# Kernel optimization log

Measured on AMD Instinct MI355X. Metric: run time of the kernel, lower is better.

## Reference

```python
import jax, jax.numpy as jnp
import numpy as np

H = 1024; NH = 16; L = 4; K = 128; N = 65536
ADIM_MOVE = 9; ADIM_TURN = 4; S = 2 * K + 2


def setup_inputs() -> dict:
    key = jax.random.key(0)
    ks = jax.random.split(key, 24)
    s = 0.02
    d = {}
    d['x'] = jax.random.normal(ks[0], (1, H), jnp.float32)
    d['memory_vectors'] = jax.random.normal(ks[1], (N, H), jnp.float32)
    d['memory_next_vectors'] = jax.random.normal(ks[2], (N, H), jnp.float32)
    d['memory_surprises'] = jax.random.uniform(ks[3], (N,), jnp.float32)
    d['memory_rewards'] = jax.random.normal(ks[4], (N,), jnp.float32)
    d['rand_noise'] = jax.random.uniform(ks[5], (N,), jnp.float32)
    d['action_idx_move'] = jax.random.randint(ks[6], (N,), 0, ADIM_MOVE)
    d['action_idx_turn'] = jax.random.randint(ks[7], (N,), 0, ADIM_TURN)
    d['start_token'] = jax.random.uniform(ks[8], (1, H)) * 2 - 1
    d['pos_emb'] = jax.random.uniform(ks[9], (S, H)) * 2 - 1
    d['in_proj_w'] = jax.random.normal(ks[10], (L, 3 * H, H)) * s
    d['in_proj_b'] = jnp.zeros((L, 3 * H))
    d['out_w'] = jax.random.normal(ks[11], (L, H, H)) * s
    d['out_b'] = jnp.zeros((L, H))
    d['ln1_w'] = jnp.ones((L, H)); d['ln1_b'] = jnp.zeros((L, H))
    d['ln2_w'] = jnp.ones((L, H)); d['ln2_b'] = jnp.zeros((L, H))
    d['ffn_w1'] = jax.random.normal(ks[12], (L, 4 * H, H)) * s
    d['ffn_b1'] = jnp.zeros((L, 4 * H))
    d['ffn_w2'] = jax.random.normal(ks[13], (L, H, 4 * H)) * s
    d['ffn_b2'] = jnp.zeros((L, H))
    d['act_move_w1'] = jax.random.normal(ks[14], (H, ADIM_MOVE)) * s
    d['act_move_b1'] = jnp.zeros((H,))
    d['act_move_w2'] = jax.random.normal(ks[15], (H, H)) * s
    d['act_move_b2'] = jnp.zeros((H,))
    d['act_turn_w1'] = jax.random.normal(ks[16], (H, ADIM_TURN)) * s
    d['act_turn_b1'] = jnp.zeros((H,))
    d['act_turn_w2'] = jax.random.normal(ks[17], (H, H)) * s
    d['act_turn_b2'] = jnp.zeros((H,))
    d['vh_w1'] = jax.random.normal(ks[18], (4 * H, H)) * s
    d['vh_b1'] = jnp.zeros((4 * H,))
    d['vh_w2'] = jax.random.normal(ks[19], (1, 4 * H)) * s
    d['vh_b2'] = jnp.zeros((1,))
    return d


def _get_scores(v):
    # tie-aware average rank / N (matches torch unique_consecutive logic)
    srt = jnp.sort(v)
    left = jnp.searchsorted(srt, v, side='left')
    right = jnp.searchsorted(srt, v, side='right')
    return ((left + right - 1).astype(v.dtype) / 2) / v.shape[0]


def _ln(x, w, b):
    m = x.mean(-1, keepdims=True)
    var = ((x - m) ** 2).mean(-1, keepdims=True)
    return (x - m) / jnp.sqrt(var + 1e-5) * w + b


def _gelu(x):
    return jax.nn.gelu(x, approximate=False)


def _mha(x, wqkv, bqkv, wo, bo, mask):
    dh = H // NH
    qkv = x @ wqkv.T + bqkv                      # [S, 3H]
    q, k, v = jnp.split(qkv, 3, axis=-1)
    q = q.reshape(-1, NH, dh); k = k.reshape(-1, NH, dh); v = v.reshape(-1, NH, dh)
    att = jnp.einsum('qhd,khd->hqk', q, k) / np.sqrt(dh).astype(np.float32)
    att = jax.nn.softmax(att + mask, axis=-1)
    o = jnp.einsum('hqk,khd->qhd', att, v).reshape(-1, H)
    return o @ wo.T + bo


def reference(x, memory_vectors, memory_next_vectors, memory_surprises, memory_rewards, rand_noise, action_idx_move, action_idx_turn, start_token, pos_emb, in_proj_w, in_proj_b, out_w, out_b, ln1_w, ln1_b, ln2_w, ln2_b, ffn_w1, ffn_b1, ffn_w2, ffn_b2, act_move_w1, act_move_b1, act_move_w2, act_move_b2, act_turn_w1, act_turn_b1, act_turn_w2, act_turn_b2, vh_w1, vh_b1, vh_w2, vh_b2):
    eps = 1e-8
    # ---- scoring (no_grad in original) ----
    xs = jax.lax.stop_gradient(x)
    xn = xs / jnp.maximum(jnp.linalg.norm(xs, axis=-1, keepdims=True), eps)
    mn = memory_vectors / jnp.maximum(jnp.linalg.norm(memory_vectors, axis=-1, keepdims=True), eps)
    sim = mn @ xn[0]                              # [N]
    scores = _get_scores(memory_surprises) ** 2 + _get_scores(sim) ** 2 + _get_scores(rand_noise) ** 2
    _, idx = jax.lax.top_k(scores, K)             # [K]
    # ---- gather memories + action one-hots ----
    sel = jax.lax.stop_gradient(memory_vectors[idx])   # [K, H]
    oh_move = jax.nn.one_hot(action_idx_move[idx], ADIM_MOVE, dtype=x.dtype)
    oh_turn = jax.nn.one_hot(action_idx_turn[idx], ADIM_TURN, dtype=x.dtype)
    av_move = _gelu(oh_move @ act_move_w1.T + act_move_b1) @ act_move_w2.T + act_move_b2
    av_turn = _gelu(oh_turn @ act_turn_w1.T + act_turn_b1) @ act_turn_w2.T + act_turn_b2
    av = (av_move + av_turn) / 2                  # mean over actions
    # interleave [v0, a0, v1, a1, ...], prepend start, append target
    vecs = jnp.stack((sel, av), axis=1).reshape(-1, H)
    vecs = jnp.concatenate((start_token, vecs, x), axis=0)   # [S, H]
    vecs = vecs + pos_emb
    mask = jnp.where(jnp.tril(jnp.ones((S, S), bool)), 0.0, -jnp.inf).astype(x.dtype)
    for l in range(L):
        vecs = vecs + _mha(_ln(vecs, ln1_w[l], ln1_b[l]), in_proj_w[l], in_proj_b[l], out_w[l], out_b[l], mask)
        h = _ln(vecs, ln2_w[l], ln2_b[l])
        vecs = vecs + _gelu(h @ ffn_w1[l].T + ffn_b1[l]) @ ffn_w2[l].T + ffn_b2[l]
    vidx = jnp.arange(K + 1) * 2 + 1
    vh_in = vecs[vidx]
    vp = _gelu(vh_in @ vh_w1.T + vh_b1) @ vh_w2.T + vh_b2   # [K+1, 1]
    sel_rewards = memory_rewards[idx]
    losses = (vp[:-1].ravel() - sel_rewards) ** 2            # mse, reduction='none'
    return (vecs[1:], memory_next_vectors[idx], vp[-1], losses, sel_rewards)
```

## Files before the change

kernel.cpp:

```cpp
#include <hip/hip_runtime.h>
#include <hip/hip_bf16.h>
#include <math.h>
#include <stdint.h>

typedef unsigned int u32;
typedef unsigned short u16;
typedef unsigned long long u64;

#define NM   65536
#define HD   1024
#define KS   128
#define SQ   258
#define NL   4
#define NBIN 65536
#define CCAP 2048

using bf16x8 = __attribute__((ext_vector_type(8))) short;
using f32x4v = __attribute__((ext_vector_type(4))) float;

struct Ctrl { u32 b1, above1, T, candcnt; };

static constexpr size_t A256(size_t x){ return (x + 255) & ~(size_t)255; }

constexpr size_t OFF_H3   = 0;
constexpr size_t OFF_C3   = OFF_H3 + (size_t)3*NBIN*4;
constexpr size_t OFF_HS   = OFF_C3 + (size_t)3*NBIN*4;
constexpr size_t ZERO_BYTES = OFF_HS + (size_t)NBIN*4;
constexpr size_t OFF_BS   = A256(ZERO_BYTES);
constexpr size_t OFF_BB   = A256(OFF_BS + 192*4);
constexpr size_t OFF_VPB  = A256(OFF_BB + 192*4);
constexpr size_t OFF_XN   = A256(OFF_VPB + 1024);
constexpr size_t OFF_P3   = A256(OFF_XN + (size_t)HD*4);
constexpr size_t OFF_K3   = A256(OFF_P3 + (size_t)3*(NBIN+1)*4);
constexpr size_t OFF_L3   = A256(OFF_K3 + (size_t)3*NM*4);
constexpr size_t OFF_KSC  = A256(OFF_L3 + (size_t)3*NM*4);
constexpr size_t OFF_CAND = A256(OFF_KSC + (size_t)NM*4);
constexpr size_t OFF_CTRL = A256(OFF_CAND + (size_t)CCAP*8);
constexpr size_t OFF_IDX  = A256(OFF_CTRL + 256);
constexpr size_t OFF_REW  = A256(OFF_IDX  + (size_t)KS*4);
constexpr size_t OFF_HM   = A256(OFF_REW  + (size_t)KS*4);
constexpr size_t OFF_HT   = A256(OFF_HM   + (size_t)KS*HD*2);
constexpr size_t OFF_VECS = A256(OFF_HT   + (size_t)KS*HD*2);
constexpr size_t OFF_LNB  = A256(OFF_VECS + (size_t)SQ*HD*4);
constexpr size_t OFF_QKV  = A256(OFF_LNB  + (size_t)SQ*HD*2);
constexpr size_t OFF_ATT  = A256(OFF_QKV  + (size_t)SQ*3*HD*4);
constexpr size_t OFF_FFH  = A256(OFF_ATT  + (size_t)SQ*HD*2);
constexpr size_t OFF_VHIN = A256(OFF_FFH  + (size_t)SQ*4*HD*2);
constexpr size_t OFF_WB   = A256(OFF_VHIN + (size_t)129*HD*2);
constexpr size_t NWELEM   = 56623104;
constexpr size_t OFF_PART = A256(OFF_WB + NWELEM*2);

constexpr size_t WB_IN = 0;
constexpr size_t WB_O  = WB_IN + (size_t)4*3*HD*HD;
constexpr size_t WB_F1 = WB_O  + (size_t)4*HD*HD;
constexpr size_t WB_F2 = WB_F1 + (size_t)4*4*HD*HD;
constexpr size_t WB_AM = WB_F2 + (size_t)4*4*HD*HD;
constexpr size_t WB_AT = WB_AM + (size_t)HD*HD;
constexpr size_t WB_VH = WB_AT + (size_t)HD*HD;

constexpr int OUT_NEXT = 257*HD;
constexpr int OUT_VP   = OUT_NEXT + KS*HD;
constexpr int OUT_LOSS = OUT_VP + 1;
constexpr int OUT_REWO = OUT_LOSS + KS;

__device__ __forceinline__ float gelu_f(float v){
  return 0.5f*v*(1.0f + erff(v*0.70710678118654752440f));
}

__device__ __forceinline__ u16 f2bf(float f){
  __hip_bfloat16 h = __float2bfloat16(f);
  u16 s;
  __builtin_memcpy(&s, &h, sizeof(u16));
  return s;
}

__device__ __forceinline__ u32 fkey(float v){
  u32 b = __float_as_uint(v);
  return (b >> 31) ? ~b : (b | 0x80000000u);
}

__device__ __forceinline__ void gload16(const u16* g, u16* l){
  __builtin_amdgcn_global_load_lds(
      (const __attribute__((address_space(1))) unsigned int*)g,
      (__attribute__((address_space(3))) unsigned int*)l, 16, 0, 0);
}

struct WSeg { const float* s; u16* d; u32 base4, end4; };
struct WCA { WSeg seg[7]; u32 tot4; };
__global__ __launch_bounds__(256) void k_wconv(WCA a){
  u32 i = blockIdx.x*256 + threadIdx.x;
  if(i >= a.tot4) return;
  #pragma unroll
  for(int j=0;j<7;++j){
    if(i < a.seg[j].end4){
      u32 off = i - a.seg[j].base4;
      float4 v = *(const float4*)&a.seg[j].s[(size_t)off*4];
      u16 r[4] = { f2bf(v.x), f2bf(v.y), f2bf(v.z), f2bf(v.w) };
      u64 pk; __builtin_memcpy(&pk, r, 8);
      *(u64*)&a.seg[j].d[(size_t)off*4] = pk;
      return;
    }
  }
}

__global__ void k_xn(const float* __restrict__ x, float* __restrict__ xn){
  __shared__ float red[256];
  int t = threadIdx.x;
  float s = 0.f;
  for(int i=t;i<HD;i+=256){ float v=x[i]; s += v*v; }
  red[t]=s; __syncthreads();
  for(int o=128;o>0;o>>=1){ if(t<o) red[t]+=red[t+o]; __syncthreads(); }
  float nrm = fmaxf(sqrtf(red[0]), 1e-8f);
  for(int i=t;i<HD;i+=256) xn[i] = x[i]/nrm;
}

__global__ __launch_bounds__(256) void k_simkey(const float* __restrict__ mv, const float* __restrict__ xn,
                                                const float* __restrict__ surp, const float* __restrict__ noise,
                                                u32* __restrict__ keys3, u32* __restrict__ hist3){
  __shared__ float xs[HD];
  int t = threadIdx.x;
  for(int i=t;i<HD;i+=256) xs[i]=xn[i];
  __syncthreads();
  int lane = t & 63, w = t >> 6;
  int row = blockIdx.x*4 + w;
  const float4* p = (const float4*)(mv + (size_t)row*HD);
  const float4* q = (const float4*)xs;
  float d=0.f, ss=0.f;
  #pragma unroll
  for(int r=0;r<4;++r){
    float4 v = p[lane + 64*r]; float4 u = q[lane + 64*r];
    d  += v.x*u.x + v.y*u.y + v.z*u.z + v.w*u.w;
    ss += v.x*v.x + v.y*v.y + v.z*v.z + v.w*v.w;
  }
  for(int off=32;off>0;off>>=1){ d += __shfl_xor(d,off,64); ss += __shfl_xor(ss,off,64); }
  if(lane==0){
    float sim = d / fmaxf(sqrtf(ss),1e-8f);
    float vals[3] = { surp[row], sim, noise[row] };
    #pragma unroll
    for(int a=0;a<3;++a){
      u32 k = fkey(vals[a]);
      keys3[(size_t)a*NM + row] = k;
      atomicAdd(&hist3[(size_t)a*NBIN + (k >> 16)], 1u);
    }
  }
}

__global__ __launch_bounds__(256) void k_scanA(const u32* __restrict__ hist3, u32* __restrict__ bsum){
  __shared__ u32 red[256];
  int blk = blockIdx.x;
  int t = threadIdx.x;
  const u32* h = hist3 + (size_t)(blk>>6)*NBIN + (size_t)(blk&63)*1024;
  u32 s = 0;
  #pragma unroll
  for(int j=0;j<4;++j) s += h[t*4+j];
  red[t]=s; __syncthreads();
  for(int o=128;o>0;o>>=1){ if(t<o) red[t]+=red[t+o]; __syncthreads(); }
  if(t==0) bsum[blk] = red[0];
}

__global__ __launch_bounds__(256) void k_scanB(const u32* __restrict__ bsum, u32* __restrict__ bbase,
                                               u32* __restrict__ pref3){
  __shared__ u32 incl[256];
  int t = threadIdx.x;
  u32 v = (t < 192) ? bsum[t] : 0u;
  incl[t] = v; __syncthreads();
  for(int off=1;off<256;off<<=1){
    u32 u = (t >= off) ? incl[t-off] : 0u;
    __syncthreads(); incl[t] += u; __syncthreads();
  }
  if(t < 192){
    int a = t >> 6;
    u32 excl_t = incl[t] - v;
    u32 excl_a = incl[a*64] - bsum[a*64];
    bbase[t] = excl_t - excl_a;
  }
  if(t < 3) pref3[(size_t)t*(NBIN+1) + NBIN] = NM;
}

__global__ __launch_bounds__(256) void k_scanC(const u32* __restrict__ hist3, const u32* __restrict__ bbase,
                                               u32* __restrict__ pref3){
  __shared__ u32 part[256];
  int blk = blockIdx.x;
  int t = threadIdx.x;
  int a = blk >> 6, c = blk & 63;
  const u32* h = hist3 + (size_t)a*NBIN + (size_t)c*1024;
  u32* pref = pref3 + (size_t)a*(NBIN+1) + (size_t)c*1024;
  u32 loc[4]; u32 s = 0;
  #pragma unroll
  for(int j=0;j<4;++j){ loc[j] = h[t*4+j]; s += loc[j]; }
  part[t] = s; __syncthreads();
  for(int off=1;off<256;off<<=1){
    u32 u = (t >= off) ? part[t-off] : 0u;
    __syncthreads(); part[t] += u; __syncthreads();
  }
  u32 run = bbase[blk] + part[t] - s;
  #pragma unroll
  for(int j=0;j<4;++j){ pref[t*4+j] = run; run += loc[j]; }
}

__global__ void k_scatter3(const u32* __restrict__ keys3, const u32* __restrict__ pref3,
                           u32* __restrict__ cnt3, u32* __restrict__ lo3){
  int i = blockIdx.x*256 + threadIdx.x;
  if(i >= NM) return;
  #pragma unroll
  for(int a=0;a<3;++a){
    u32 k = keys3[(size_t)a*NM + i];
    u32 b = k >> 16;
    u32 pos = pref3[(size_t)a*(NBIN+1) + b] + atomicAdd(&cnt3[(size_t)a*NBIN + b], 1u);
    lo3[(size_t)a*NM + pos] = k & 0xFFFFu;
  }
}

__global__ void k_rank3score(const u32* __restrict__ keys3, const u32* __restrict__ pref3,
                             const u32* __restrict__ lo3, u32* __restrict__ keysS, u32* __restrict__ histS){
  int i = blockIdx.x*256 + threadIdx.x;
  if(i >= NM) return;
  float rr[3];
  #pragma unroll
  for(int a=0;a<3;++a){
    u32 k = keys3[(size_t)a*NM + i];
    u32 b = k >> 16, my = k & 0xFFFFu;
    const u32* pref = pref3 + (size_t)a*(NBIN+1);
    const u32* lo = lo3 + (size_t)a*NM;
    u32 s = pref[b], e = pref[b+1];
    u32 nl = 0, ne = 0;
    for(u32 j=s;j<e;++j){ u32 u = lo[j]; nl += (u < my); ne += (u == my); }
    u32 left = s + nl, right = left + ne;
    rr[a] = (float)(left + right - 1) * (1.0f/131072.0f);
  }
  float sc = __fadd_rn(__fadd_rn(__fmul_rn(rr[0],rr[0]), __fmul_rn(rr[1],rr[1])), __fmul_rn(rr[2],rr[2]));
  u32 k = __float_as_uint(sc);
  keysS[i] = k;
  atomicAdd(&histS[k >> 16], 1u);
}

__global__ __launch_bounds__(1024) void k_sel1(const u32* __restrict__ hist, Ctrl* ctrl){
  __shared__ u32 part[1024];
  int t = threadIdx.x;
  u32 base = t*64, s = 0;
  for(int j=0;j<64;++j) s += hist[base+j];
  part[t] = s; __syncthreads();
  for(int off=1;off<1024;off<<=1){
    u32 v = (t+off < 1024) ? part[t+off] : 0u;
    __syncthreads(); part[t] += v; __syncthreads();
  }
  u32 above = part[t] - s;
  if(above < (u32)KS && above + s >= (u32)KS){
    u32 cum = above;
    for(int j=63;j>=0;--j){
      u32 c = hist[base+j];
      if(cum + c >= (u32)KS){ ctrl->T = (u32)(base+j) << 16; ctrl->candcnt = 0; break; }
      cum += c;
    }
  }
}

__global__ void k_collect(const u32* __restrict__ keys, Ctrl* ctrl, u64* __restrict__ cand){
  int i = blockIdx.x*256 + threadIdx.x;
  if(i >= NM) return;
  u32 k = keys[i];
  if(k >= ctrl->T){
    u32 p = atomicAdd(&ctrl->candcnt, 1u);
    if(p < (u32)CCAP) cand[p] = ((u64)(~k) << 32) | (u32)i;
  }
}

__global__ __launch_bounds__(1024) void k_sortsel(const u64* __restrict__ cand, const Ctrl* ctrl, int* __restrict__ idx){
  __shared__ u64 sm[CCAP];
  int t = threadIdx.x;
  u32 n = ctrl->candcnt; if(n > (u32)CCAP) n = CCAP;
  for(int i=t;i<CCAP;i+=1024) sm[i] = (i < (int)n) ? cand[i] : 0xFFFFFFFFFFFFFFFFull;
  __syncthreads();
  for(int k=2;k<=CCAP;k<<=1){
    for(int j=k>>1;j>0;j>>=1){
      for(int i=t;i<CCAP;i+=1024){
        int ixj = i ^ j;
        if(ixj > i){
          bool up = ((i & k) == 0);
          u64 a = sm[i], b = sm[ixj];
          if((a > b) == up){ sm[i] = b; sm[ixj] = a; }
        }
      }
      __syncthreads();
    }
  }
  if(t < KS) idx[t] = (int)(sm[t] & 0xFFFFFFFFu);
}

__global__ void k_gather(const int* __restrict__ idx,
                         const float* __restrict__ mv, const float* __restrict__ mnv,
                         const float* __restrict__ mrew,
                         const int* __restrict__ aim, const int* __restrict__ ait,
                         const float* __restrict__ amw1, const float* __restrict__ amb1,
                         const float* __restrict__ atw1, const float* __restrict__ atb1,
                         const float* __restrict__ start, const float* __restrict__ x,
                         const float* __restrict__ pos,
                         float* __restrict__ vecs, float* __restrict__ outnext,
                         u16* __restrict__ hm, u16* __restrict__ ht,
                         float* __restrict__ rew, float* __restrict__ outrew){
  int k = blockIdx.x;
  int t = threadIdx.x;
  if(k < KS){
    int row = idx[k];
    const float* a = mv  + (size_t)row*HD;
    const float* b = mnv + (size_t)row*HD;
    const float* pz = pos + (size_t)(2*k+1)*HD;
    float* vr = vecs + (size_t)(2*k+1)*HD;
    for(int c=t;c<HD;c+=256){
      vr[c] = a[c] + pz[c];
      outnext[(size_t)k*HD+c] = b[c];
    }
    int am = aim[row], at = ait[row];
    for(int j=t;j<HD;j+=256){
      hm[(size_t)k*HD+j] = f2bf(gelu_f(amw1[(size_t)j*9 + am] + amb1[j]));
      ht[(size_t)k*HD+j] = f2bf(gelu_f(atw1[(size_t)j*4 + at] + atb1[j]));
    }
    if(t == 0){ float r = mrew[row]; rew[k] = r; outrew[k] = r; }
  } else {
    for(int c=t;c<HD;c+=256){
      vecs[c] = start[c] + pos[c];
      vecs[(size_t)(SQ-1)*HD + c] = x[c] + pos[(size_t)(SQ-1)*HD + c];
    }
  }
}

__device__ __forceinline__ void gemm_body(u16* As, u16* Bs, const u16* __restrict__ A, const u16* __restrict__ B,
        float* __restrict__ P, int M, int N, int K, int S, int nbm, int lda, int tile){
  int bm = (tile % nbm) * 64;
  int tmp = tile / nbm;
  int z  = tmp % S;
  int bn = (tmp / S) * 64;
  int Ks = K / S, kbeg = z*Ks;
  int nk = Ks >> 5;

  int t = threadIdx.x, lane = t & 63, w = t >> 6;
  int srow = w*16 + (lane >> 2);
  int clog = (lane & 3) ^ ((srow >> 1) & 3);
  const u16* ga = A + (size_t)(bm + srow)*lda + kbeg + clog*8;
  const u16* gb = B + (size_t)(bn + srow)*K  + kbeg + clog*8;
  u16* la = As + w*512;
  u16* lb = Bs + w*512;

  int wm = (w >> 1)*32, wn = (w & 1)*32;
  int lr = lane & 15, lg = lane >> 4;
  int r0 = wm + lr, r1 = r0 + 16;
  int c0 = wn + lr, c1 = c0 + 16;
  int aoff0 = r0*32 + ((lg ^ ((r0>>1)&3))*8);
  int aoff1 = r1*32 + ((lg ^ ((r1>>1)&3))*8);
  int boff0 = c0*32 + ((lg ^ ((c0>>1)&3))*8);
  int boff1 = c1*32 + ((lg ^ ((c1>>1)&3))*8);

  f32x4v acc00 = {0,0,0,0}, acc01 = {0,0,0,0}, acc10 = {0,0,0,0}, acc11 = {0,0,0,0};

  gload16(ga, la);
  gload16(gb, lb);
  ga += 32; gb += 32;
  __syncthreads();

  for(int kk = 0; kk < nk; ++kk){
    int cur = (kk & 1) * 2048;
    if(kk + 1 < nk){
      int nxt = 2048 - cur;
      gload16(ga, la + nxt);
      gload16(gb, lb + nxt);
      ga += 32; gb += 32;
    }
    bf16x8 a0 = *(const bf16x8*)&As[cur + aoff0];
    bf16x8 a1 = *(const bf16x8*)&As[cur + aoff1];
    bf16x8 b0 = *(const bf16x8*)&Bs[cur + boff0];
    bf16x8 b1 = *(const bf16x8*)&Bs[cur + boff1];
    acc00 = __builtin_amdgcn_mfma_f32_16x16x32_bf16(a0, b0, acc00, 0, 0, 0);
    acc01 = __builtin_amdgcn_mfma_f32_16x16x32_bf16(a0, b1, acc01, 0, 0, 0);
    acc10 = __builtin_amdgcn_mfma_f32_16x16x32_bf16(a1, b0, acc10, 0, 0, 0);
    acc11 = __builtin_amdgcn_mfma_f32_16x16x32_bf16(a1, b1, acc11, 0, 0, 0);
    __syncthreads();
  }

  size_t zbase = (size_t)z * (size_t)M;
  #pragma unroll
  for(int r=0;r<4;++r){
    int row0 = bm + wm + lg*4 + r;
    int row1 = row0 + 16;
    int cc0 = bn + wn + lr, cc1 = cc0 + 16;
    if(row0 < M){
      P[(zbase+row0)*N + cc0] = acc00[r];
      P[(zbase+row0)*N + cc1] = acc01[r];
    }
    if(row1 < M){
      P[(zbase+row1)*N + cc0] = acc10[r];
      P[(zbase+row1)*N + cc1] = acc11[r];
    }
  }
}

__global__ __launch_bounds__(256) void k_gemm(const u16* __restrict__ A, const u16* __restrict__ B,
        float* __restrict__ P, int M, int N, int K, int S, int nbm, int lda){
  __shared__ u16 As[4096];
  __shared__ u16 Bs[4096];
  u32 nwg = gridDim.x, orig = blockIdx.x;
  u32 swz = (orig & 7)*(nwg >> 3) + (orig >> 3);
  gemm_body(As, Bs, A, B, P, M, N, K, S, nbm, lda, (int)swz);
}

__global__ __launch_bounds__(256) void k_actgemm(const u16* __restrict__ hm, const u16* __restrict__ ht,
        const u16* __restrict__ amw2, const u16* __restrict__ atw2,
        float* __restrict__ part, float* __restrict__ part2){
  __shared__ u16 As[4096];
  __shared__ u16 Bs[4096];
  int which = blockIdx.x >> 8, tile = blockIdx.x & 255;
  gemm_body(As, Bs, which ? ht : hm, which ? atw2 : amw2, which ? part2 : part,
            KS, HD, HD, 8, 2, HD, tile);
}

template<int S_, int ACT, bool BF>
__global__ __launch_bounds__(256) void k_finS(const float* __restrict__ P, const float* __restrict__ bias,
                                              float* __restrict__ C, u16* __restrict__ Cb, int MN4, int Nd){
  int i4 = blockIdx.x*256 + threadIdx.x;
  if(i4 >= MN4) return;
  size_t off = (size_t)i4*4;
  size_t MN = (size_t)MN4*4;
  float4 v = *(const float4*)&P[off];
  #pragma unroll
  for(int z=1;z<S_;++z){
    float4 q = *(const float4*)&P[(size_t)z*MN + off];
    v.x += q.x; v.y += q.y; v.z += q.z; v.w += q.w;
  }
  int j = (i4 % (Nd/4))*4;
  float4 b4 = *(const float4*)&bias[j];
  v.x += b4.x; v.y += b4.y; v.z += b4.z; v.w += b4.w;
  if(ACT == 1){ v.x = gelu_f(v.x); v.y = gelu_f(v.y); v.z = gelu_f(v.z); v.w = gelu_f(v.w); }
  if(BF){
    u16 r[4] = { f2bf(v.x), f2bf(v.y), f2bf(v.z), f2bf(v.w) };
    u64 pk; __builtin_memcpy(&pk, r, 8);
    *(u64*)&Cb[off] = pk;
  } else {
    *(float4*)&C[off] = v;
  }
}

template<int S_, bool LN>
__global__ __launch_bounds__(256) void k_finrow(const float* __restrict__ P, const float* __restrict__ bias,
                                                float* __restrict__ vecs, const float* __restrict__ lw,
                                                const float* __restrict__ lb, u16* __restrict__ lnb,
                                                float* __restrict__ outp, u16* __restrict__ vhin){
  __shared__ float red[256];
  int row = blockIdx.x, t = threadIdx.x;
  int j = t*4;
  float4 v = *(const float4*)&P[(size_t)row*HD + j];
  #pragma unroll
  for(int z=1;z<S_;++z){
    float4 p = *(const float4*)&P[((size_t)z*SQ + row)*HD + j];
    v.x += p.x; v.y += p.y; v.z += p.z; v.w += p.w;
  }
  float4 b4 = *(const float4*)&bias[j];
  float4 r4 = *(const float4*)&vecs[(size_t)row*HD + j];
  v.x += b4.x + r4.x; v.y += b4.y + r4.y; v.z += b4.z + r4.z; v.w += b4.w + r4.w;
  *(float4*)&vecs[(size_t)row*HD + j] = v;
  if(LN){
    red[t] = v.x+v.y+v.z+v.w; __syncthreads();
    for(int o=128;o>0;o>>=1){ if(t<o) red[t]+=red[t+o]; __syncthreads(); }
    float m = red[0]*(1.0f/HD); __syncthreads();
    float dx=v.x-m, dy=v.y-m, dz=v.z-m, dw=v.w-m;
    red[t] = dx*dx+dy*dy+dz*dz+dw*dw; __syncthreads();
    for(int o=128;o>0;o>>=1){ if(t<o) red[t]+=red[t+o]; __syncthreads(); }
    float den = sqrtf(red[0]*(1.0f/HD) + 1e-5f);
    float4 w4 = *(const float4*)&lw[j];
    float4 lb4 = *(const float4*)&lb[j];
    u16 r[4] = { f2bf(dx/den*w4.x + lb4.x), f2bf(dy/den*w4.y + lb4.y),
                 f2bf(dz/den*w4.z + lb4.z), f2bf(dw/den*w4.w + lb4.w) };
    u64 pk; __builtin_memcpy(&pk, r, 8);
    *(u64*)&lnb[(size_t)row*HD + j] = pk;
  } else {
    if(row >= 1) *(float4*)&outp[(size_t)(row-1)*HD + j] = v;
    if(row & 1){
      int vr = (row-1) >> 1;
      u16 r[4] = { f2bf(v.x), f2bf(v.y), f2bf(v.z), f2bf(v.w) };
      u64 pk; __builtin_memcpy(&pk, r, 8);
      *(u64*)&vhin[(size_t)vr*HD + j] = pk;
    }
  }
}

__global__ __launch_bounds__(256) void k_finavln(const float* __restrict__ Pm, const float* __restrict__ Pt,
                                                 const float* __restrict__ bm_, const float* __restrict__ bt_,
                                                 const float* __restrict__ pos, float* __restrict__ vecs,
                                                 const float* __restrict__ lw, const float* __restrict__ lb,
                                                 u16* __restrict__ lnb){
  __shared__ float red[256];
  int row = blockIdx.x, t = threadIdx.x;
  int j = t*4;
  float4 v;
  if(row >= 2 && row <= 256 && ((row & 1) == 0)){
    int k = (row-2) >> 1;
    float4 s = {0,0,0,0};
    #pragma unroll
    for(int z=0;z<8;++z){
      float4 a = *(const float4*)&Pm[((size_t)z*KS + k)*HD + j];
      float4 b = *(const float4*)&Pt[((size_t)z*KS + k)*HD + j];
      s.x += a.x+b.x; s.y += a.y+b.y; s.z += a.z+b.z; s.w += a.w+b.w;
    }
    float4 bm4 = *(const float4*)&bm_[j];
    float4 bt4 = *(const float4*)&bt_[j];
    float4 p4 = *(const float4*)&pos[(size_t)row*HD + j];
    v.x = 0.5f*(s.x + bm4.x + bt4.x) + p4.x;
    v.y = 0.5f*(s.y + bm4.y + bt4.y) + p4.y;
    v.z = 0.5f*(s.z + bm4.z + bt4.z) + p4.z;
    v.w = 0.5f*(s.w + bm4.w + bt4.w) + p4.w;
    *(float4*)&vecs[(size_t)row*HD + j] = v;
  } else {
    v = *(const float4*)&vecs[(size_t)row*HD + j];
  }
  red[t] = v.x+v.y+v.z+v.w; __syncthreads();
  for(int o=128;o>0;o>>=1){ if(t<o) red[t]+=red[t+o]; __syncthreads(); }
  float m = red[0]*(1.0f/HD); __syncthreads();
  float dx=v.x-m, dy=v.y-m, dz=v.z-m, dw=v.w-m;
  red[t] = dx*dx+dy*dy+dz*dz+dw*dw; __syncthreads();
  for(int o=128;o>0;o>>=1){ if(t<o) red[t]+=red[t+o]; __syncthreads(); }
  float den = sqrtf(red[0]*(1.0f/HD) + 1e-5f);
  float4 w4 = *(const float4*)&lw[j];
  float4 lb4 = *(const float4*)&lb[j];
  u16 r[4] = { f2bf(dx/den*w4.x + lb4.x), f2bf(dy/den*w4.y + lb4.y),
               f2bf(dz/den*w4.z + lb4.z), f2bf(dw/den*w4.w + lb4.w) };
  u64 pk; __builtin_memcpy(&pk, r, 8);
  *(u64*)&lnb[(size_t)row*HD + j] = pk;
}

__global__ void k_attn(const float* __restrict__ qkv, u16* __restrict__ outp){
  __shared__ float qv[64];
  __shared__ float p[SQ];
  __shared__ float red[256];
  int q = blockIdx.x, h = blockIdx.y, t = threadIdx.x;
  if(t < 64) qv[t] = qkv[(size_t)q*3072 + h*64 + t];
  __syncthreads();
  int nk = q + 1;
  float lmax = -1e30f;
  for(int j=t;j<nk;j+=256){
    const float* kr = qkv + (size_t)j*3072 + 1024 + h*64;
    float d = 0.f;
    for(int c=0;c<64;++c) d += qv[c]*kr[c];
    d *= 0.125f;
    p[j] = d;
    lmax = fmaxf(lmax, d);
  }
  red[t] = lmax; __syncthreads();
  for(int o=128;o>0;o>>=1){ if(t<o) red[t] = fmaxf(red[t], red[t+o]); __syncthreads(); }
  float m = red[0];
  __syncthreads();
  float lsum = 0.f;
  for(int j=t;j<nk;j+=256){ float e = expf(p[j]-m); p[j] = e; lsum += e; }
  red[t] = lsum; __syncthreads();
  for(int o=128;o>0;o>>=1){ if(t<o) red[t] += red[t+o]; __syncthreads(); }
  float inv = 1.0f/red[0];
  __syncthreads();
  int d = t & 63, g = t >> 6;
  float acc = 0.f;
  for(int j=g;j<nk;j+=4) acc += p[j]*qkv[(size_t)j*3072 + 2048 + h*64 + d];
  red[t] = acc; __syncthreads();
  if(g == 0){
    float o4 = red[d] + red[64+d] + red[128+d] + red[192+d];
    outp[(size_t)q*HD + h*64 + d] = f2bf(o4*inv);
  }
}

__global__ __launch_bounds__(256) void k_vpfin(const float* __restrict__ P, const float* __restrict__ vb1,
                                               const float* __restrict__ vw2, float* __restrict__ vp){
  __shared__ float red[256];
  int r = blockIdx.x, t = threadIdx.x;
  float s = 0.f;
  for(int c=t;c<4096;c+=256){
    float v = P[(size_t)r*4096 + c];
    #pragma unroll
    for(int z=1;z<4;++z) v += P[((size_t)z*129 + r)*4096 + c];
    s += gelu_f(v + vb1[c]) * vw2[c];
  }
  red[t]=s; __syncthreads();
  for(int o=128;o>0;o>>=1){ if(t<o) red[t]+=red[t+o]; __syncthreads(); }
  if(t == 0) vp[r] = red[0];
}

__global__ void k_outsmall(const float* __restrict__ vp, const float* __restrict__ b2,
                           const float* __restrict__ rew, float* __restrict__ outp){
  int t = threadIdx.x;
  float bb = b2[0];
  if(t == 0) outp[OUT_VP] = vp[KS] + bb;
  if(t < KS){
    float d = (vp[t] + bb) - rew[t];
    outp[OUT_LOSS + t] = d*d;
    outp[OUT_REWO + t] = rew[t];
  }
}

extern "C" void kernel_launch(void* const* d_in, const int* in_sizes, int n_in,
                              void* d_out, int out_size, void* d_ws, size_t ws_size,
                              hipStream_t stream){
  const float* x     = (const float*)d_in[0];
  const float* mv    = (const float*)d_in[1];
  const float* mnv   = (const float*)d_in[2];
  const float* surp  = (const float*)d_in[3];
  const float* mrew  = (const float*)d_in[4];
  const float* noise = (const float*)d_in[5];
  const int*   aim   = (const int*)d_in[6];
  const int*   ait   = (const int*)d_in[7];
  const float* start = (const float*)d_in[8];
  const float* pos   = (const float*)d_in[9];
  const float* inW = (const float*)d_in[10]; const float* inB = (const float*)d_in[11];
  const float* oW  = (const float*)d_in[12]; const float* oB  = (const float*)d_in[13];
  const float* l1w = (const float*)d_in[14]; const float* l1b = (const float*)d_in[15];
  const float* l2w = (const float*)d_in[16]; const float* l2b = (const float*)d_in[17];
  const float* f1w = (const float*)d_in[18]; const float* f1b = (const float*)d_in[19];
  const float* f2w = (const float*)d_in[20]; const float* f2b = (const float*)d_in[21];
  const float* amw1= (const float*)d_in[22]; const float* amb1= (const float*)d_in[23];
  const float* amw2= (const float*)d_in[24]; const float* amb2= (const float*)d_in[25];
  const float* atw1= (const float*)d_in[26]; const float* atb1= (const float*)d_in[27];
  const float* atw2= (const float*)d_in[28]; const float* atb2= (const float*)d_in[29];
  const float* vw1 = (const float*)d_in[30]; const float* vb1 = (const float*)d_in[31];
  const float* vw2 = (const float*)d_in[32]; const float* vb2 = (const float*)d_in[33];

  float* out = (float*)d_out;
  char* ws = (char*)d_ws;
  u32*  hist3 = (u32*)(ws+OFF_H3);
  u32*  cnt3  = (u32*)(ws+OFF_C3);
  u32*  histS = (u32*)(ws+OFF_HS);
  u32*  bsum  = (u32*)(ws+OFF_BS);
  u32*  bbase = (u32*)(ws+OFF_BB);
  float* vp   = (float*)(ws+OFF_VPB);
  float* xn   = (float*)(ws+OFF_XN);
  u32*  pref3 = (u32*)(ws+OFF_P3);
  u32*  keys3 = (u32*)(ws+OFF_K3);
  u32*  lo3   = (u32*)(ws+OFF_L3);
  u32*  keysS = (u32*)(ws+OFF_KSC);
  u64*  cand  = (u64*)(ws+OFF_CAND);
  Ctrl* ctrl  = (Ctrl*)(ws+OFF_CTRL);
  int*  idxb  = (int*)(ws+OFF_IDX);
  float* rew  = (float*)(ws+OFF_REW);
  u16*  hm    = (u16*)(ws+OFF_HM);
  u16*  ht    = (u16*)(ws+OFF_HT);
  float* vecs = (float*)(ws+OFF_VECS);
  u16*  lnb   = (u16*)(ws+OFF_LNB);
  float* qkvb = (float*)(ws+OFF_QKV);
  u16*  attn  = (u16*)(ws+OFF_ATT);
  u16*  ffh   = (u16*)(ws+OFF_FFH);
  u16*  vhin  = (u16*)(ws+OFF_VHIN);
  u16*  wb    = (u16*)(ws+OFF_WB);
  float* part = (float*)(ws+OFF_PART);
  float* part2= part + (size_t)8*KS*HD;

  u16* inW_bf = wb + WB_IN;
  u16* oW_bf  = wb + WB_O;
  u16* f1w_bf = wb + WB_F1;
  u16* f2w_bf = wb + WB_F2;
  u16* am_bf  = wb + WB_AM;
  u16* at_bf  = wb + WB_AT;
  u16* vh_bf  = wb + WB_VH;

  dim3 b256(256);
  int gN = NM/256;

  (void)hipMemsetAsync(ws, 0, ZERO_BYTES, stream);

  {
    WCA a;
    const float* srcs[7] = { inW, oW, f1w, f2w, amw2, atw2, vw1 };
    u16* dsts[7] = { inW_bf, oW_bf, f1w_bf, f2w_bf, am_bf, at_bf, vh_bf };
    u32 sizes4[7] = { 4*3*HD*HD/4, 4*HD*HD/4, 4*4*HD*HD/4, 4*4*HD*HD/4, HD*HD/4, HD*HD/4, 4*HD*HD/4 };
    u32 cum = 0;
    for(int j=0;j<7;++j){
      a.seg[j].s = srcs[j]; a.seg[j].d = dsts[j];
      a.seg[j].base4 = cum; cum += sizes4[j]; a.seg[j].end4 = cum;
    }
    a.tot4 = cum;
    hipLaunchKernelGGL(k_wconv, dim3((cum + 255)/256), b256, 0, stream, a);
  }

  hipLaunchKernelGGL(k_xn, dim3(1), b256, 0, stream, x, xn);
  hipLaunchKernelGGL(k_simkey, dim3(NM/4), b256, 0, stream, mv, xn, surp, noise, keys3, hist3);
  hipLaunchKernelGGL(k_scanA, dim3(192), b256, 0, stream, hist3, bsum);
  hipLaunchKernelGGL(k_scanB, dim3(1), b256, 0, stream, bsum, bbase, pref3);
  hipLaunchKernelGGL(k_scanC, dim3(192), b256, 0, stream, hist3, bbase, pref3);
  hipLaunchKernelGGL(k_scatter3, dim3(gN), b256, 0, stream, keys3, pref3, cnt3, lo3);
  hipLaunchKernelGGL(k_rank3score, dim3(gN), b256, 0, stream, keys3, pref3, lo3, keysS, histS);
  hipLaunchKernelGGL(k_sel1, dim3(1), dim3(1024), 0, stream, histS, ctrl);
  hipLaunchKernelGGL(k_collect, dim3(gN), b256, 0, stream, keysS, ctrl, cand);
  hipLaunchKernelGGL(k_sortsel, dim3(1), dim3(1024), 0, stream, cand, ctrl, idxb);

  hipLaunchKernelGGL(k_gather, dim3(KS+1), b256, 0, stream, idxb, mv, mnv, mrew, aim, ait,
                     amw1, amb1, atw1, atb1, start, x, pos,
                     vecs, out + OUT_NEXT, hm, ht, rew, out + OUT_REWO);
  hipLaunchKernelGGL(k_actgemm, dim3(512), b256, 0, stream, hm, ht, am_bf, at_bf, part, part2);
  hipLaunchKernelGGL(k_finavln, dim3(SQ), b256, 0, stream, part, part2, amb2, atb2, pos, vecs, l1w, l1b, lnb);

  for(int l=0;l<NL;++l){
    hipLaunchKernelGGL(k_gemm, dim3(480), b256, 0, stream, lnb, inW_bf + (size_t)l*3*HD*HD, part, SQ, 3*HD, HD, 2, 5, HD);
    hipLaunchKernelGGL((k_finS<2,0,false>), dim3(774), b256, 0, stream, part, inB + (size_t)l*3*HD, qkvb, (u16*)nullptr, SQ*3*HD/4, 3*HD);
    hipLaunchKernelGGL(k_attn, dim3(SQ, 16), b256, 0, stream, qkvb, attn);
    hipLaunchKernelGGL(k_gemm, dim3(640), b256, 0, stream, attn, oW_bf + (size_t)l*HD*HD, part, SQ, HD, HD, 8, 5, HD);
    hipLaunchKernelGGL((k_finrow<8,true>), dim3(SQ), b256, 0, stream, part, oB + (size_t)l*HD, vecs,
                       l2w + (size_t)l*HD, l2b + (size_t)l*HD, lnb, (float*)nullptr, (u16*)nullptr);
    hipLaunchKernelGGL(k_gemm, dim3(640), b256, 0, stream, lnb, f1w_bf + (size_t)l*4*HD*HD, part, SQ, 4*HD, HD, 2, 5, HD);
    hipLaunchKernelGGL((k_finS<2,1,true>), dim3(1032), b256, 0, stream, part, f1b + (size_t)l*4*HD, (float*)nullptr, ffh, SQ*4*HD/4, 4*HD);
    hipLaunchKernelGGL(k_gemm, dim3(640), b256, 0, stream, ffh, f2w_bf + (size_t)l*HD*4*HD, part, SQ, HD, 4*HD, 8, 5, 4*HD);
    if(l < NL-1)
      hipLaunchKernelGGL((k_finrow<8,true>), dim3(SQ), b256, 0, stream, part, f2b + (size_t)l*HD, vecs,
                         l1w + (size_t)(l+1)*HD, l1b + (size_t)(l+1)*HD, lnb, (float*)nullptr, (u16*)nullptr);
    else
      hipLaunchKernelGGL((k_finrow<8,false>), dim3(SQ), b256, 0, stream, part, f2b + (size_t)l*HD, vecs,
                         (const float*)nullptr, (const float*)nullptr, (u16*)nullptr, out, vhin);
  }

  hipLaunchKernelGGL(k_gemm, dim3(768), b256, 0, stream, vhin, vh_bf, part, KS+1, 4*HD, HD, 4, 3, HD);
  hipLaunchKernelGGL(k_vpfin, dim3(KS+1), b256, 0, stream, part, vb1, vw2, vp);
  hipLaunchKernelGGL(k_outsmall, dim3(1), b256, 0, stream, vp, vb2, rew, out);
}
```

Before: 947.5 us.

## Fuse small kernels, store split-K partials and qkv in bf16, fold memset into wconv

Several small launches are merged: x-normalisation goes into simkey, scanB into scanC, sel1/collect/sortsel into one selection kernel, and outsmall into vpfin. The workspace memset is replaced by zeroing inside the weight-conversion kernel. Split-K GEMM partials and the qkv buffer are now stored as bf16 instead of fp32, roughly halving that memory traffic at the cost of extra rounding in the partial sums. The gather copies and simkey are also vectorised or processed two rows per wave.

```diff
diff --git a/kernel.cpp b/kernel.cpp
--- a/kernel.cpp
+++ b/kernel.cpp
@@ -18,32 +18,26 @@
 using bf16x8 = __attribute__((ext_vector_type(8))) short;
 using f32x4v = __attribute__((ext_vector_type(4))) float;
 
-struct Ctrl { u32 b1, above1, T, candcnt; };
-
 static constexpr size_t A256(size_t x){ return (x + 255) & ~(size_t)255; }
 
 constexpr size_t OFF_H3   = 0;
 constexpr size_t OFF_C3   = OFF_H3 + (size_t)3*NBIN*4;
 constexpr size_t OFF_HS   = OFF_C3 + (size_t)3*NBIN*4;
 constexpr size_t ZERO_BYTES = OFF_HS + (size_t)NBIN*4;
+constexpr u32 ZBLK = 1792;
 constexpr size_t OFF_BS   = A256(ZERO_BYTES);
-constexpr size_t OFF_BB   = A256(OFF_BS + 192*4);
-constexpr size_t OFF_VPB  = A256(OFF_BB + 192*4);
-constexpr size_t OFF_XN   = A256(OFF_VPB + 1024);
-constexpr size_t OFF_P3   = A256(OFF_XN + (size_t)HD*4);
+constexpr size_t OFF_P3   = A256(OFF_BS + 192*4);
 constexpr size_t OFF_K3   = A256(OFF_P3 + (size_t)3*(NBIN+1)*4);
 constexpr size_t OFF_L3   = A256(OFF_K3 + (size_t)3*NM*4);
 constexpr size_t OFF_KSC  = A256(OFF_L3 + (size_t)3*NM*4);
-constexpr size_t OFF_CAND = A256(OFF_KSC + (size_t)NM*4);
-constexpr size_t OFF_CTRL = A256(OFF_CAND + (size_t)CCAP*8);
-constexpr size_t OFF_IDX  = A256(OFF_CTRL + 256);
+constexpr size_t OFF_IDX  = A256(OFF_KSC + (size_t)NM*4);
 constexpr size_t OFF_REW  = A256(OFF_IDX  + (size_t)KS*4);
 constexpr size_t OFF_HM   = A256(OFF_REW  + (size_t)KS*4);
 constexpr size_t OFF_HT   = A256(OFF_HM   + (size_t)KS*HD*2);
 constexpr size_t OFF_VECS = A256(OFF_HT   + (size_t)KS*HD*2);
 constexpr size_t OFF_LNB  = A256(OFF_VECS + (size_t)SQ*HD*4);
 constexpr size_t OFF_QKV  = A256(OFF_LNB  + (size_t)SQ*HD*2);
-constexpr size_t OFF_ATT  = A256(OFF_QKV  + (size_t)SQ*3*HD*4);
+constexpr size_t OFF_ATT  = A256(OFF_QKV  + (size_t)SQ*3*HD*2);
 constexpr size_t OFF_FFH  = A256(OFF_ATT  + (size_t)SQ*HD*2);
 constexpr size_t OFF_VHIN = A256(OFF_FFH  + (size_t)SQ*4*HD*2);
 constexpr size_t OFF_WB   = A256(OFF_VHIN + (size_t)129*HD*2);
@@ -63,15 +57,34 @@
 constexpr int OUT_LOSS = OUT_VP + 1;
 constexpr int OUT_REWO = OUT_LOSS + KS;
 
+struct Ctrl { u32 b1, above1, T, candcnt; };
+
 __device__ __forceinline__ float gelu_f(float v){
   return 0.5f*v*(1.0f + erff(v*0.70710678118654752440f));
 }
 
 __device__ __forceinline__ u16 f2bf(float f){
   __hip_bfloat16 h = __float2bfloat16(f);
-  u16 s;
-  __builtin_memcpy(&s, &h, sizeof(u16));
+  u16 s; __builtin_memcpy(&s, &h, sizeof(u16));
   return s;
+}
+
+__device__ __forceinline__ float bf2f(u16 v){ return __uint_as_float(((u32)v) << 16); }
+
+__device__ __forceinline__ float4 unpk4(u64 pk){
+  u32 lo = (u32)pk, hi = (u32)(pk >> 32);
+  float4 v;
+  v.x = __uint_as_float(lo << 16);
+  v.y = __uint_as_float(lo & 0xFFFF0000u);
+  v.z = __uint_as_float(hi << 16);
+  v.w = __uint_as_float(hi & 0xFFFF0000u);
+  return v;
+}
+
+__device__ __forceinline__ u64 pk4(float4 v){
+  u16 r[4] = { f2bf(v.x), f2bf(v.y), f2bf(v.z), f2bf(v.w) };
+  u64 pk; __builtin_memcpy(&pk, r, 8);
+  return pk;
 }
 
 __device__ __forceinline__ u32 fkey(float v){
@@ -86,8 +99,9 @@
 }
 
 struct WSeg { const float* s; u16* d; u32 base4, end4; };
-struct WCA { WSeg seg[7]; u32 tot4; };
+struct WCA { WSeg seg[7]; u32 tot4; u32* z; };
 __global__ __launch_bounds__(256) void k_wconv(WCA a){
+  if(blockIdx.x < ZBLK) a.z[blockIdx.x*256 + threadIdx.x] = 0u;
   u32 i = blockIdx.x*256 + threadIdx.x;
   if(i >= a.tot4) return;
   #pragma unroll
@@ -95,15 +109,16 @@
     if(i < a.seg[j].end4){
       u32 off = i - a.seg[j].base4;
       float4 v = *(const float4*)&a.seg[j].s[(size_t)off*4];
-      u16 r[4] = { f2bf(v.x), f2bf(v.y), f2bf(v.z), f2bf(v.w) };
-      u64 pk; __builtin_memcpy(&pk, r, 8);
-      *(u64*)&a.seg[j].d[(size_t)off*4] = pk;
+      *(u64*)&a.seg[j].d[(size_t)off*4] = pk4(v);
       return;
     }
   }
 }
 
-__global__ void k_xn(const float* __restrict__ x, float* __restrict__ xn){
+__global__ __launch_bounds__(256) void k_simkey(const float* __restrict__ mv, const float* __restrict__ x,
+                                                const float* __restrict__ surp, const float* __restrict__ noise,
+                                                u32* __restrict__ keys3, u32* __restrict__ hist3){
+  __shared__ float xs[HD];
   __shared__ float red[256];
   int t = threadIdx.x;
   float s = 0.f;
@@ -111,36 +126,31 @@
   red[t]=s; __syncthreads();
   for(int o=128;o>0;o>>=1){ if(t<o) red[t]+=red[t+o]; __syncthreads(); }
   float nrm = fmaxf(sqrtf(red[0]), 1e-8f);
-  for(int i=t;i<HD;i+=256) xn[i] = x[i]/nrm;
-}
-
-__global__ __launch_bounds__(256) void k_simkey(const float* __restrict__ mv, const float* __restrict__ xn,
-                                                const float* __restrict__ surp, const float* __restrict__ noise,
-                                                u32* __restrict__ keys3, u32* __restrict__ hist3){
-  __shared__ float xs[HD];
-  int t = threadIdx.x;
-  for(int i=t;i<HD;i+=256) xs[i]=xn[i];
+  for(int i=t;i<HD;i+=256) xs[i] = x[i]/nrm;
   __syncthreads();
   int lane = t & 63, w = t >> 6;
-  int row = blockIdx.x*4 + w;
-  const float4* p = (const float4*)(mv + (size_t)row*HD);
-  const float4* q = (const float4*)xs;
-  float d=0.f, ss=0.f;
-  #pragma unroll
-  for(int r=0;r<4;++r){
-    float4 v = p[lane + 64*r]; float4 u = q[lane + 64*r];
-    d  += v.x*u.x + v.y*u.y + v.z*u.z + v.w*u.w;
-    ss += v.x*v.x + v.y*v.y + v.z*v.z + v.w*v.w;
-  }
-  for(int off=32;off>0;off>>=1){ d += __shfl_xor(d,off,64); ss += __shfl_xor(ss,off,64); }
-  if(lane==0){
-    float sim = d / fmaxf(sqrtf(ss),1e-8f);
-    float vals[3] = { surp[row], sim, noise[row] };
+  #pragma unroll
+  for(int rep=0;rep<2;++rep){
+    int row = blockIdx.x*8 + rep*4 + w;
+    const float4* p = (const float4*)(mv + (size_t)row*HD);
+    const float4* q = (const float4*)xs;
+    float d=0.f, ss=0.f;
     #pragma unroll
-    for(int a=0;a<3;++a){
-      u32 k = fkey(vals[a]);
-      keys3[(size_t)a*NM + row] = k;
-      atomicAdd(&hist3[(size_t)a*NBIN + (k >> 16)], 1u);
+    for(int r=0;r<4;++r){
+      float4 v = p[lane + 64*r]; float4 u = q[lane + 64*r];
+      d  += v.x*u.x + v.y*u.y + v.z*u.z + v.w*u.w;
+      ss += v.x*v.x + v.y*v.y + v.z*v.z + v.w*v.w;
+    }
+    for(int off=32;off>0;off>>=1){ d += __shfl_xor(d,off,64); ss += __shfl_xor(ss,off,64); }
+    if(lane==0){
+      float sim = d / fmaxf(sqrtf(ss),1e-8f);
+      float vals[3] = { surp[row], sim, noise[row] };
+      #pragma unroll
+      for(int a=0;a<3;++a){
+        u32 k = fkey(vals[a]);
+        keys3[(size_t)a*NM + row] = k;
+        atomicAdd(&hist3[(size_t)a*NBIN + (k >> 16)], 1u);
+      }
     }
   }
 }
@@ -158,31 +168,14 @@
   if(t==0) bsum[blk] = red[0];
 }
 
-__global__ __launch_bounds__(256) void k_scanB(const u32* __restrict__ bsum, u32* __restrict__ bbase,
-                                               u32* __restrict__ pref3){
-  __shared__ u32 incl[256];
-  int t = threadIdx.x;
-  u32 v = (t < 192) ? bsum[t] : 0u;
-  incl[t] = v; __syncthreads();
-  for(int off=1;off<256;off<<=1){
-    u32 u = (t >= off) ? incl[t-off] : 0u;
-    __syncthreads(); incl[t] += u; __syncthreads();
-  }
-  if(t < 192){
-    int a = t >> 6;
-    u32 excl_t = incl[t] - v;
-    u32 excl_a = incl[a*64] - bsum[a*64];
-    bbase[t] = excl_t - excl_a;
-  }
-  if(t < 3) pref3[(size_t)t*(NBIN+1) + NBIN] = NM;
-}
-
-__global__ __launch_bounds__(256) void k_scanC(const u32* __restrict__ hist3, const u32* __restrict__ bbase,
+__global__ __launch_bounds__(256) void k_scanC(const u32* __restrict__ hist3, const u32* __restrict__ bsum,
                                                u32* __restrict__ pref3){
   __shared__ u32 part[256];
   int blk = blockIdx.x;
   int t = threadIdx.x;
   int a = blk >> 6, c = blk & 63;
+  u32 base = 0;
+  for(int j=0;j<c;++j) base += bsum[a*64 + j];
   const u32* h = hist3 + (size_t)a*NBIN + (size_t)c*1024;
   u32* pref = pref3 + (size_t)a*(NBIN+1) + (size_t)c*1024;
   u32 loc[4]; u32 s = 0;
@@ -193,9 +186,10 @@
     u32 u = (t >= off) ? part[t-off] : 0u;
     __syncthreads(); part[t] += u; __syncthreads();
   }
-  u32 run = bbase[blk] + part[t] - s;
+  u32 run = base + part[t] - s;
   #pragma unroll
   for(int j=0;j<4;++j){ pref[t*4+j] = run; run += loc[j]; }
+  if(c == 63 && t == 255) pref3[(size_t)a*(NBIN+1) + NBIN] = NM;
 }
 
 __global__ void k_scatter3(const u32* __restrict__ keys3, const u32* __restrict__ pref3,
@@ -234,11 +228,14 @@
   atomicAdd(&histS[k >> 16], 1u);
 }
 
-__global__ __launch_bounds__(1024) void k_sel1(const u32* __restrict__ hist, Ctrl* ctrl){
+__global__ __launch_bounds__(1024) void k_selsort(const u32* __restrict__ histS, const u32* __restrict__ keysS,
+                                                  int* __restrict__ idx){
   __shared__ u32 part[1024];
+  __shared__ u64 sm[CCAP];
+  __shared__ u32 thrT, cnt;
   int t = threadIdx.x;
   u32 base = t*64, s = 0;
-  for(int j=0;j<64;++j) s += hist[base+j];
+  for(int j=0;j<64;++j) s += histS[base+j];
   part[t] = s; __syncthreads();
   for(int off=1;off<1024;off<<=1){
     u32 v = (t+off < 1024) ? part[t+off] : 0u;
@@ -248,28 +245,23 @@
   if(above < (u32)KS && above + s >= (u32)KS){
     u32 cum = above;
     for(int j=63;j>=0;--j){
-      u32 c = hist[base+j];
-      if(cum + c >= (u32)KS){ ctrl->T = (u32)(base+j) << 16; ctrl->candcnt = 0; break; }
+      u32 c = histS[base+j];
+      if(cum + c >= (u32)KS){ thrT = (u32)(base+j) << 16; cnt = 0; break; }
       cum += c;
     }
   }
-}
-
-__global__ void k_collect(const u32* __restrict__ keys, Ctrl* ctrl, u64* __restrict__ cand){
-  int i = blockIdx.x*256 + threadIdx.x;
-  if(i >= NM) return;
-  u32 k = keys[i];
-  if(k >= ctrl->T){
-    u32 p = atomicAdd(&ctrl->candcnt, 1u);
-    if(p < (u32)CCAP) cand[p] = ((u64)(~k) << 32) | (u32)i;
-  }
-}
-
-__global__ __launch_bounds__(1024) void k_sortsel(const u64* __restrict__ cand, const Ctrl* ctrl, int* __restrict__ idx){
-  __shared__ u64 sm[CCAP];
-  int t = threadIdx.x;
-  u32 n = ctrl->candcnt; if(n > (u32)CCAP) n = CCAP;
-  for(int i=t;i<CCAP;i+=1024) sm[i] = (i < (int)n) ? cand[i] : 0xFFFFFFFFFFFFFFFFull;
+  __syncthreads();
+  u32 T = thrT;
+  for(int i=t;i<NM;i+=1024){
+    u32 k = keysS[i];
+    if(k >= T){
+      u32 p = atomicAdd(&cnt, 1u);
+      if(p < (u32)CCAP) sm[p] = ((u64)(~k) << 32) | (u32)i;
+    }
+  }
+  __syncthreads();
+  u32 n = cnt; if(n > (u32)CCAP) n = CCAP;
+  for(int i=t;i<CCAP;i+=1024) if(i >= (int)n) sm[i] = 0xFFFFFFFFFFFFFFFFull;
   __syncthreads();
   for(int k=2;k<=CCAP;k<<=1){
     for(int j=k>>1;j>0;j>>=1){
@@ -302,14 +294,14 @@
   int t = threadIdx.x;
   if(k < KS){
     int row = idx[k];
-    const float* a = mv  + (size_t)row*HD;
-    const float* b = mnv + (size_t)row*HD;
-    const float* pz = pos + (size_t)(2*k+1)*HD;
-    float* vr = vecs + (size_t)(2*k+1)*HD;
-    for(int c=t;c<HD;c+=256){
-      vr[c] = a[c] + pz[c];
-      outnext[(size_t)k*HD+c] = b[c];
-    }
+    const float4* a = (const float4*)(mv  + (size_t)row*HD);
+    const float4* b = (const float4*)(mnv + (size_t)row*HD);
+    const float4* pz = (const float4*)(pos + (size_t)(2*k+1)*HD);
+    float4* vr = (float4*)(vecs + (size_t)(2*k+1)*HD);
+    float4* on = (float4*)(outnext + (size_t)k*HD);
+    float4 av = a[t], bv = b[t], pv = pz[t];
+    av.x += pv.x; av.y += pv.y; av.z += pv.z; av.w += pv.w;
+    vr[t] = av; on[t] = bv;
     int am = aim[row], at = ait[row];
     for(int j=t;j<HD;j+=256){
       hm[(size_t)k*HD+j] = f2bf(gelu_f(amw1[(size_t)j*9 + am] + amb1[j]));
@@ -317,15 +309,20 @@
     }
     if(t == 0){ float r = mrew[row]; rew[k] = r; outrew[k] = r; }
   } else {
-    for(int c=t;c<HD;c+=256){
-      vecs[c] = start[c] + pos[c];
-      vecs[(size_t)(SQ-1)*HD + c] = x[c] + pos[(size_t)(SQ-1)*HD + c];
-    }
+    const float4* st = (const float4*)start;
+    const float4* xx = (const float4*)x;
+    const float4* p0 = (const float4*)pos;
+    const float4* p1 = (const float4*)(pos + (size_t)(SQ-1)*HD);
+    float4 v0 = st[t], v1 = xx[t], q0 = p0[t], q1 = p1[t];
+    v0.x += q0.x; v0.y += q0.y; v0.z += q0.z; v0.w += q0.w;
+    v1.x += q1.x; v1.y += q1.y; v1.z += q1.z; v1.w += q1.w;
+    ((float4*)vecs)[t] = v0;
+    ((float4*)(vecs + (size_t)(SQ-1)*HD))[t] = v1;
   }
 }
 
 __device__ __forceinline__ void gemm_body(u16* As, u16* Bs, const u16* __restrict__ A, const u16* __restrict__ B,
-        float* __restrict__ P, int M, int N, int K, int S, int nbm, int lda, int tile){
+        u16* __restrict__ P, int M, int N, int K, int S, int nbm, int lda, int tile){
   int bm = (tile % nbm) * 64;
   int tmp = tile / nbm;
   int z  = tmp % S;
@@ -383,18 +380,18 @@
     int row1 = row0 + 16;
     int cc0 = bn + wn + lr, cc1 = cc0 + 16;
     if(row0 < M){
-      P[(zbase+row0)*N + cc0] = acc00[r];
-      P[(zbase+row0)*N + cc1] = acc01[r];
+      P[(zbase+row0)*N + cc0] = f2bf(acc00[r]);
+      P[(zbase+row0)*N + cc1] = f2bf(acc01[r]);
     }
     if(row1 < M){
-      P[(zbase+row1)*N + cc0] = acc10[r];
-      P[(zbase+row1)*N + cc1] = acc11[r];
+      P[(zbase+row1)*N + cc0] = f2bf(acc10[r]);
+      P[(zbase+row1)*N + cc1] = f2bf(acc11[r]);
     }
   }
 }
 
 __global__ __launch_bounds__(256) void k_gemm(const u16* __restrict__ A, const u16* __restrict__ B,
-        float* __restrict__ P, int M, int N, int K, int S, int nbm, int lda){
+        u16* __restrict__ P, int M, int N, int K, int S, int nbm, int lda){
   __shared__ u16 As[4096];
   __shared__ u16 Bs[4096];
   u32 nwg = gridDim.x, orig = blockIdx.x;
@@ -404,7 +401,7 @@
 
 __global__ __launch_bounds__(256) void k_actgemm(const u16* __restrict__ hm, const u16* __restrict__ ht,
         const u16* __restrict__ amw2, const u16* __restrict__ atw2,
-        float* __restrict__ part, float* __restrict__ part2){
+        u16* __restrict__ part, u16* __restrict__ part2){
   __shared__ u16 As[4096];
   __shared__ u16 Bs[4096];
   int which = blockIdx.x >> 8, tile = blockIdx.x & 255;
@@ -412,44 +409,39 @@
             KS, HD, HD, 8, 2, HD, tile);
 }
 
-template<int S_, int ACT, bool BF>
-__global__ __launch_bounds__(256) void k_finS(const float* __restrict__ P, const float* __restrict__ bias,
+template<int S_, int ACT, bool BFOUT>
+__global__ __launch_bounds__(256) void k_finS(const u16* __restrict__ P, const float* __restrict__ bias,
                                               float* __restrict__ C, u16* __restrict__ Cb, int MN4, int Nd){
   int i4 = blockIdx.x*256 + threadIdx.x;
   if(i4 >= MN4) return;
   size_t off = (size_t)i4*4;
   size_t MN = (size_t)MN4*4;
-  float4 v = *(const float4*)&P[off];
+  float4 v = unpk4(*(const u64*)&P[off]);
   #pragma unroll
   for(int z=1;z<S_;++z){
-    float4 q = *(const float4*)&P[(size_t)z*MN + off];
+    float4 q = unpk4(*(const u64*)&P[(size_t)z*MN + off]);
     v.x += q.x; v.y += q.y; v.z += q.z; v.w += q.w;
   }
   int j = (i4 % (Nd/4))*4;
   float4 b4 = *(const float4*)&bias[j];
   v.x += b4.x; v.y += b4.y; v.z += b4.z; v.w += b4.w;
   if(ACT == 1){ v.x = gelu_f(v.x); v.y = gelu_f(v.y); v.z = gelu_f(v.z); v.w = gelu_f(v.w); }
-  if(BF){
-    u16 r[4] = { f2bf(v.x), f2bf(v.y), f2bf(v.z), f2bf(v.w) };
-    u64 pk; __builtin_memcpy(&pk, r, 8);
-    *(u64*)&Cb[off] = pk;
-  } else {
-    *(float4*)&C[off] = v;
-  }
+  if(BFOUT) *(u64*)&Cb[off] = pk4(v);
+  else      *(float4*)&C[off] = v;
 }
 
 template<int S_, bool LN>
-__global__ __launch_bounds__(256) void k_finrow(const float* __restrict__ P, const float* __restrict__ bias,
+__global__ __launch_bounds__(256) void k_finrow(const u16* __restrict__ P, const float* __restrict__ bias,
                                                 float* __restrict__ vecs, const float* __restrict__ lw,
                                                 const float* __restrict__ lb, u16* __restrict__ lnb,
                                                 float* __restrict__ outp, u16* __restrict__ vhin){
   __shared__ float red[256];
   int row = blockIdx.x, t = threadIdx.x;
   int j = t*4;
-  float4 v = *(const float4*)&P[(size_t)row*HD + j];
+  float4 v = unpk4(*(const u64*)&P[(size_t)row*HD + j]);
   #pragma unroll
   for(int z=1;z<S_;++z){
-    float4 p = *(const float4*)&P[((size_t)z*SQ + row)*HD + j];
+    float4 p = unpk4(*(const u64*)&P[((size_t)z*SQ + row)*HD + j]);
     v.x += p.x; v.y += p.y; v.z += p.z; v.w += p.w;
   }
   float4 b4 = *(const float4*)&bias[j];
@@ -466,22 +458,20 @@
     float den = sqrtf(red[0]*(1.0f/HD) + 1e-5f);
     float4 w4 = *(const float4*)&lw[j];
     float4 lb4 = *(const float4*)&lb[j];
-    u16 r[4] = { f2bf(dx/den*w4.x + lb4.x), f2bf(dy/den*w4.y + lb4.y),
-                 f2bf(dz/den*w4.z + lb4.z), f2bf(dw/den*w4.w + lb4.w) };
-    u64 pk; __builtin_memcpy(&pk, r, 8);
-    *(u64*)&lnb[(size_t)row*HD + j] = pk;
+    float4 o4;
+    o4.x = dx/den*w4.x + lb4.x; o4.y = dy/den*w4.y + lb4.y;
+    o4.z = dz/den*w4.z + lb4.z; o4.w = dw/den*w4.w + lb4.w;
+    *(u64*)&lnb[(size_t)row*HD + j] = pk4(o4);
   } else {
     if(row >= 1) *(float4*)&outp[(size_t)(row-1)*HD + j] = v;
     if(row & 1){
       int vr = (row-1) >> 1;
-      u16 r[4] = { f2bf(v.x), f2bf(v.y), f2bf(v.z), f2bf(v.w) };
-      u64 pk; __builtin_memcpy(&pk, r, 8);
-      *(u64*)&vhin[(size_t)vr*HD + j] = pk;
-    }
-  }
-}
-
-__global__ __launch_bounds__(256) void k_finavln(const float* __restrict__ Pm, const float* __restrict__ Pt,
+      *(u64*)&vhin[(size_t)vr*HD + j] = pk4(v);
+    }
+  }
+}
+
+__global__ __launch_bounds__(256) void k_finavln(const u16* __restrict__ Pm, const u16* __restrict__ Pt,
                                                  const float* __restrict__ bm_, const float* __restrict__ bt_,
                                                  const float* __restrict__ pos, float* __restrict__ vecs,
                                                  const float* __restrict__ lw, const float* __restrict__ lb,
@@ -495,8 +485,8 @@
     float4 s = {0,0,0,0};
     #pragma unroll
     for(int z=0;z<8;++z){
-      float4 a = *(const float4*)&Pm[((size_t)z*KS + k)*HD + j];
-      float4 b = *(const float4*)&Pt[((size_t)z*KS + k)*HD + j];
+      float4 a = unpk4(*(const u64*)&Pm[((size_t)z*KS + k)*HD + j]);
+      float4 b = unpk4(*(const u64*)&Pt[((size_t)z*KS + k)*HD + j]);
       s.x += a.x+b.x; s.y += a.y+b.y; s.z += a.z+b.z; s.w += a.w+b.w;
     }
     float4 bm4 = *(const float4*)&bm_[j];
@@ -519,25 +509,30 @@
   float den = sqrtf(red[0]*(1.0f/HD) + 1e-5f);
   float4 w4 = *(const float4*)&lw[j];
   float4 lb4 = *(const float4*)&lb[j];
-  u16 r[4] = { f2bf(dx/den*w4.x + lb4.x), f2bf(dy/den*w4.y + lb4.y),
-               f2bf(dz/den*w4.z + lb4.z), f2bf(dw/den*w4.w + lb4.w) };
-  u64 pk; __builtin_memcpy(&pk, r, 8);
-  *(u64*)&lnb[(size_t)row*HD + j] = pk;
-}
-
-__global__ void k_attn(const float* __restrict__ qkv, u16* __restrict__ outp){
+  float4 o4;
+  o4.x = dx/den*w4.x + lb4.x; o4.y = dy/den*w4.y + lb4.y;
+  o4.z = dz/den*w4.z + lb4.z; o4.w = dw/den*w4.w + lb4.w;
+  *(u64*)&lnb[(size_t)row*HD + j] = pk4(o4);
+}
+
+__global__ void k_attn(const u16* __restrict__ qkv, u16* __restrict__ outp){
   __shared__ float qv[64];
   __shared__ float p[SQ];
   __shared__ float red[256];
   int q = blockIdx.x, h = blockIdx.y, t = threadIdx.x;
-  if(t < 64) qv[t] = qkv[(size_t)q*3072 + h*64 + t];
+  if(t < 64) qv[t] = bf2f(qkv[(size_t)q*3072 + h*64 + t]);
   __syncthreads();
   int nk = q + 1;
   float lmax = -1e30f;
   for(int j=t;j<nk;j+=256){
-    const float* kr = qkv + (size_t)j*3072 + 1024 + h*64;
+    const u32* kr = (const u32*)(qkv + (size_t)j*3072 + 1024 + h*64);
     float d = 0.f;
-    for(int c=0;c<64;++c) d += qv[c]*kr[c];
+    #pragma unroll
+    for(int c2=0;c2<32;++c2){
+      u32 pk = kr[c2];
+      d += qv[c2*2]   * __uint_as_float(pk << 16);
+      d += qv[c2*2+1] * __uint_as_float(pk & 0xFFFF0000u);
+    }
     d *= 0.125f;
     p[j] = d;
     lmax = fmaxf(lmax, d);
@@ -554,7 +549,7 @@
   __syncthreads();
   int d = t & 63, g = t >> 6;
   float acc = 0.f;
-  for(int j=g;j<nk;j+=4) acc += p[j]*qkv[(size_t)j*3072 + 2048 + h*64 + d];
+  for(int j=g;j<nk;j+=4) acc += p[j]*bf2f(qkv[(size_t)j*3072 + 2048 + h*64 + d]);
   red[t] = acc; __syncthreads();
   if(g == 0){
     float o4 = red[d] + red[64+d] + red[128+d] + red[192+d];
@@ -562,31 +557,30 @@
   }
 }
 
-__global__ __launch_bounds__(256) void k_vpfin(const float* __restrict__ P, const float* __restrict__ vb1,
-                                               const float* __restrict__ vw2, float* __restrict__ vp){
+__global__ __launch_bounds__(256) void k_vpfin(const u16* __restrict__ P, const float* __restrict__ vb1,
+                                               const float* __restrict__ vw2, const float* __restrict__ vb2,
+                                               const float* __restrict__ rew, float* __restrict__ outp){
   __shared__ float red[256];
   int r = blockIdx.x, t = threadIdx.x;
   float s = 0.f;
-  for(int c=t;c<4096;c+=256){
-    float v = P[(size_t)r*4096 + c];
+  for(int c4=t;c4<1024;c4+=256){
+    float4 v = unpk4(*(const u64*)&P[(size_t)r*4096 + c4*4]);
     #pragma unroll
-    for(int z=1;z<4;++z) v += P[((size_t)z*129 + r)*4096 + c];
-    s += gelu_f(v + vb1[c]) * vw2[c];
+    for(int z=1;z<4;++z){
+      float4 q = unpk4(*(const u64*)&P[((size_t)z*129 + r)*4096 + c4*4]);
+      v.x += q.x; v.y += q.y; v.z += q.z; v.w += q.w;
+    }
+    float4 b4 = *(const float4*)&vb1[c4*4];
+    float4 w4 = *(const float4*)&vw2[c4*4];
+    s += gelu_f(v.x + b4.x)*w4.x + gelu_f(v.y + b4.y)*w4.y
+       + gelu_f(v.z + b4.z)*w4.z + gelu_f(v.w + b4.w)*w4.w;
   }
   red[t]=s; __syncthreads();
   for(int o=128;o>0;o>>=1){ if(t<o) red[t]+=red[t+o]; __syncthreads(); }
-  if(t == 0) vp[r] = red[0];
-}
-
-__global__ void k_outsmall(const float* __restrict__ vp, const float* __restrict__ b2,
-                           const float* __restrict__ rew, float* __restrict__ outp){
-  int t = threadIdx.x;
-  float bb = b2[0];
-  if(t == 0) outp[OUT_VP] = vp[KS] + bb;
-  if(t < KS){
-    float d = (vp[t] + bb) - rew[t];
-    outp[OUT_LOSS + t] = d*d;
-    outp[OUT_REWO + t] = rew[t];
+  if(t == 0){
+    float val = red[0] + vb2[0];
+    if(r == KS) outp[OUT_VP] = val;
+    else { float d = val - rew[r]; outp[OUT_LOSS + r] = d*d; }
   }
 }
 
@@ -622,28 +616,23 @@
   u32*  cnt3  = (u32*)(ws+OFF_C3);
   u32*  histS = (u32*)(ws+OFF_HS);
   u32*  bsum  = (u32*)(ws+OFF_BS);
-  u32*  bbase = (u32*)(ws+OFF_BB);
-  float* vp   = (float*)(ws+OFF_VPB);
-  float* xn   = (float*)(ws+OFF_XN);
   u32*  pref3 = (u32*)(ws+OFF_P3);
   u32*  keys3 = (u32*)(ws+OFF_K3);
   u32*  lo3   = (u32*)(ws+OFF_L3);
   u32*  keysS = (u32*)(ws+OFF_KSC);
-  u64*  cand  = (u64*)(ws+OFF_CAND);
-  Ctrl* ctrl  = (Ctrl*)(ws+OFF_CTRL);
   int*  idxb  = (int*)(ws+OFF_IDX);
   float* rew  = (float*)(ws+OFF_REW);
   u16*  hm    = (u16*)(ws+OFF_HM);
   u16*  ht    = (u16*)(ws+OFF_HT);
   float* vecs = (float*)(ws+OFF_VECS);
   u16*  lnb   = (u16*)(ws+OFF_LNB);
-  float* qkvb = (float*)(ws+OFF_QKV);
+  u16*  qkvb  = (u16*)(ws+OFF_QKV);
   u16*  attn  = (u16*)(ws+OFF_ATT);
   u16*  ffh   = (u16*)(ws+OFF_FFH);
   u16*  vhin  = (u16*)(ws+OFF_VHIN);
   u16*  wb    = (u16*)(ws+OFF_WB);
-  float* part = (float*)(ws+OFF_PART);
-  float* part2= part + (size_t)8*KS*HD;
+  u16*  part  = (u16*)(ws+OFF_PART);
+  u16*  part2 = part + (size_t)8*KS*HD;
 
   u16* inW_bf = wb + WB_IN;
   u16* oW_bf  = wb + WB_O;
@@ -655,8 +644,6 @@
 
   dim3 b256(256);
   int gN = NM/256;
-
-  (void)hipMemsetAsync(ws, 0, ZERO_BYTES, stream);
 
   {
     WCA a;
@@ -669,19 +656,16 @@
       a.seg[j].base4 = cum; cum += sizes4[j]; a.seg[j].end4 = cum;
     }
     a.tot4 = cum;
+    a.z = (u32*)ws;
     hipLaunchKernelGGL(k_wconv, dim3((cum + 255)/256), b256, 0, stream, a);
   }
 
-  hipLaunchKernelGGL(k_xn, dim3(1), b256, 0, stream, x, xn);
-  hipLaunchKernelGGL(k_simkey, dim3(NM/4), b256, 0, stream, mv, xn, surp, noise, keys3, hist3);
+  hipLaunchKernelGGL(k_simkey, dim3(NM/8), b256, 0, stream, mv, x, surp, noise, keys3, hist3);
   hipLaunchKernelGGL(k_scanA, dim3(192), b256, 0, stream, hist3, bsum);
-  hipLaunchKernelGGL(k_scanB, dim3(1), b256, 0, stream, bsum, bbase, pref3);
-  hipLaunchKernelGGL(k_scanC, dim3(192), b256, 0, stream, hist3, bbase, pref3);
+  hipLaunchKernelGGL(k_scanC, dim3(192), b256, 0, stream, hist3, bsum, pref3);
   hipLaunchKernelGGL(k_scatter3, dim3(gN), b256, 0, stream, keys3, pref3, cnt3, lo3);
   hipLaunchKernelGGL(k_rank3score, dim3(gN), b256, 0, stream, keys3, pref3, lo3, keysS, histS);
-  hipLaunchKernelGGL(k_sel1, dim3(1), dim3(1024), 0, stream, histS, ctrl);
-  hipLaunchKernelGGL(k_collect, dim3(gN), b256, 0, stream, keysS, ctrl, cand);
-  hipLaunchKernelGGL(k_sortsel, dim3(1), dim3(1024), 0, stream, cand, ctrl, idxb);
+  hipLaunchKernelGGL(k_selsort, dim3(1), dim3(1024), 0, stream, histS, keysS, idxb);
 
   hipLaunchKernelGGL(k_gather, dim3(KS+1), b256, 0, stream, idxb, mv, mnv, mrew, aim, ait,
                      amw1, amb1, atw1, atb1, start, x, pos,
@@ -691,7 +675,7 @@
 
   for(int l=0;l<NL;++l){
     hipLaunchKernelGGL(k_gemm, dim3(480), b256, 0, stream, lnb, inW_bf + (size_t)l*3*HD*HD, part, SQ, 3*HD, HD, 2, 5, HD);
-    hipLaunchKernelGGL((k_finS<2,0,false>), dim3(774), b256, 0, stream, part, inB + (size_t)l*3*HD, qkvb, (u16*)nullptr, SQ*3*HD/4, 3*HD);
+    hipLaunchKernelGGL((k_finS<2,0,true>), dim3(774), b256, 0, stream, part, inB + (size_t)l*3*HD, (float*)nullptr, qkvb, SQ*3*HD/4, 3*HD);
     hipLaunchKernelGGL(k_attn, dim3(SQ, 16), b256, 0, stream, qkvb, attn);
     hipLaunchKernelGGL(k_gemm, dim3(640), b256, 0, stream, attn, oW_bf + (size_t)l*HD*HD, part, SQ, HD, HD, 8, 5, HD);
     hipLaunchKernelGGL((k_finrow<8,true>), dim3(SQ), b256, 0, stream, part, oB + (size_t)l*HD, vecs,
@@ -708,6 +692,5 @@
   }
 
   hipLaunchKernelGGL(k_gemm, dim3(768), b256, 0, stream, vhin, vh_bf, part, KS+1, 4*HD, HD, 4, 3, HD);
-  hipLaunchKernelGGL(k_vpfin, dim3(KS+1), b256, 0, stream, part, vb1, vw2, vp);
-  hipLaunchKernelGGL(k_outsmall, dim3(1), b256, 0, stream, vp, vb2, rew, out);
-}
+  hipLaunchKernelGGL(k_vpfin, dim3(KS+1), b256, 0, stream, part, vb1, vw2, vb2, rew, out);
+}
```

New measurement: 883.0 us. 6.8% less time.
